# Kernel tuning notes

Measured on AMD Instinct MI355X. Metric: run time of the kernel, lower is better.

The kernel has to match this reference:

```python
import jax, jax.numpy as jnp
import numpy as np

DIM = 512
N_HEADS = 8
N_KV_HEADS = 4
HEAD_DIM = DIM // N_HEADS  # 64
N_REP = N_HEADS // N_KV_HEADS  # 2
THETA = 10000.0
EPS_RMS = 1e-6
EPS_Z = 1e-6


def setup_inputs() -> dict:
    key = jax.random.key(0)
    ks = jax.random.split(key, 6)
    s = 1.0 / np.sqrt(DIM)
    return {
        "x": jax.random.normal(ks[0], (4, 8192, DIM), dtype=jnp.float32),
        "norm_w": jnp.ones((DIM,), dtype=jnp.float32),
        "wq": jax.random.normal(ks[1], (DIM, DIM), dtype=jnp.float32) * s,
        "wk": jax.random.normal(ks[2], (N_KV_HEADS * HEAD_DIM, DIM), dtype=jnp.float32) * s,
        "wv": jax.random.normal(ks[3], (N_KV_HEADS * HEAD_DIM, DIM), dtype=jnp.float32) * s,
        "wo": jax.random.normal(ks[4], (DIM, DIM), dtype=jnp.float32) * s,
    }


def _rope_cos_sin(seq_len, head_dim):
    # freqs_cis = polar(1, t * theta^(-2i/d))
    inv = 1.0 / (THETA ** (jnp.arange(0, head_dim, 2, dtype=jnp.float32) / head_dim))
    ang = jnp.arange(seq_len, dtype=jnp.float32)[:, None] * inv[None, :]  # (S, d/2)
    return jnp.cos(ang), jnp.sin(ang)


def _apply_rope(t, cos, sin):
    # t: (B, S, H, d); complex rotation on consecutive pairs
    B, S, H, d = t.shape
    tr = t.reshape(B, S, H, d // 2, 2)
    xr, xi = tr[..., 0], tr[..., 1]
    c = cos[None, :, None, :]  # (1, S, 1, d/2)
    s = sin[None, :, None, :]
    out = jnp.stack([xr * c - xi * s, xr * s + xi * c], axis=-1)
    return out.reshape(B, S, H, d)


def _forward(x, norm_w, wq, wk, wv, wo):
    B, S, _ = x.shape
    # RMSNorm
    x = x * jax.lax.rsqrt(jnp.mean(x * x, axis=-1, keepdims=True) + EPS_RMS) * norm_w
    xq = (x @ wq.T).reshape(B, S, N_HEADS, HEAD_DIM)
    xk = (x @ wk.T).reshape(B, S, N_KV_HEADS, HEAD_DIM)
    xv = (x @ wv.T).reshape(B, S, N_KV_HEADS, HEAD_DIM)
    cos, sin = _rope_cos_sin(S, HEAD_DIM)
    xq = _apply_rope(xq, cos, sin)
    xk = _apply_rope(xk, cos, sin)
    # repeat_kv: (B,S,Hkv,d) -> (B,S,Hkv*n_rep,d)
    keys = jnp.repeat(xk, N_REP, axis=2)
    values = jnp.repeat(xv, N_REP, axis=2)
    # to (B, H, S, d)
    Q = jnp.transpose(xq, (0, 2, 1, 3))
    K = jnp.transpose(keys, (0, 2, 1, 3))
    V = jnp.transpose(values, (0, 2, 1, 3))
    phi = lambda t: jax.nn.elu(t) + 1.0
    Q_lin, K_lin = phi(Q), phi(K)
    # Faithful to source: elementwise product reduced over s -> (B,H,d)
    KV = jnp.einsum('bhsd,bhsd->bhd', K_lin, V)
    K_sum = K_lin.sum(axis=2)  # (B,H,d)
    Z = jnp.einsum('bhsd,bhd->bhs', Q_lin, K_sum)[..., None]  # (B,H,S,1)
    Y = Q_lin * KV[:, :, None, :] / (Z + EPS_Z)  # (B,H,S,d)
    Y = jnp.transpose(Y, (0, 2, 1, 3)).reshape(B, S, N_HEADS * HEAD_DIM)
    return Y @ wo.T


def reference(x, norm_w, wq, wk, wv, wo):
    return _forward(x, norm_w, wq, wk, wv, wo)
```

## Files before the change

### kernel.cpp

```cpp
#include <hip/hip_runtime.h>
#include <cmath>

typedef __attribute__((ext_vector_type(8))) short short8;
typedef __attribute__((ext_vector_type(4))) float floatx4;

#define T_TOK 32768
#define DIMK 512

__device__ __forceinline__ unsigned short f2bf(float f) {
  union { float f; unsigned int u; } v; v.f = f;
  unsigned int r = (v.u + 0x7fffu + ((v.u >> 16) & 1u)) >> 16;
  return (unsigned short)r;
}
__device__ __forceinline__ float bf2f(unsigned short h) {
  union { unsigned int u; float f; } v; v.u = ((unsigned int)h) << 16;
  return v.f;
}

__device__ __forceinline__ void gload_lds16(const unsigned short* g, unsigned short* ldsbase) {
  __builtin_amdgcn_global_load_lds(
      (const __attribute__((address_space(1))) unsigned int*)g,
      (__attribute__((address_space(3))) unsigned int*)ldsbase, 16, 0, 0);
}

__global__ __launch_bounds__(256) void k_prep(const float* __restrict__ x,
    const float* __restrict__ norm_w, const float* __restrict__ wq,
    const float* __restrict__ wk, const float* __restrict__ wv,
    const float* __restrict__ wo, unsigned short* __restrict__ Wb,
    unsigned short* __restrict__ wob, float2* __restrict__ rope,
    float* __restrict__ KVz, unsigned short* __restrict__ xn) {
  if (blockIdx.x < 2048) {
    int i = blockIdx.x * 256 + threadIdx.x;
    float v;
    if (i < 262144) {
      v = wq[i];
    } else {
      int R = i >> 9, col = i & 511;
      int h = (R - 512) >> 7, rem = (R - 512) & 127;
      if (rem < 64) v = wk[(h * 64 + rem) * 512 + col];
      else          v = wv[(h * 64 + rem - 64) * 512 + col];
    }
    Wb[i] = f2bf(v);
    if (i < 262144) {
      wob[i] = f2bf(wo[i]);
      int s = i >> 5, m = i & 31;
      const double c0 = 0.74989420933245582;
      double c1 = c0 * c0, c2 = c1 * c1, c3 = c2 * c2, c4 = c3 * c3;
      double p = 1.0;
      if (m & 1)  p *= c0;
      if (m & 2)  p *= c1;
      if (m & 4)  p *= c2;
      if (m & 8)  p *= c3;
      if (m & 16) p *= c4;
      double ang = (double)s * p;
      const double TWO_PI = 6.2831853071795864769;
      double q = rint(ang * (1.0 / TWO_PI));
      double r = fma(-q, TWO_PI, ang);
      float rf = (float)r;
      rope[i] = make_float2(cosf(rf), sinf(rf));
    }
    if (i < 2048) KVz[i] = 0.f;
  } else {
    int bid = blockIdx.x - 2048;
    int wave = threadIdx.x >> 6, lane = threadIdx.x & 63;
    size_t t0 = ((size_t)bid * 4 + wave) * 4;
    const float4* wr = (const float4*)norm_w;
    float4 w0 = wr[lane * 2], w1 = wr[lane * 2 + 1];
    float4 a[4], b[4];
    #pragma unroll
    for (int j = 0; j < 4; j++) {
      const float4* xr = (const float4*)(x + (t0 + j) * DIMK);
      a[j] = xr[lane * 2];
      b[j] = xr[lane * 2 + 1];
    }
    #pragma unroll
    for (int j = 0; j < 4; j++) {
      float ss = a[j].x * a[j].x + a[j].y * a[j].y + a[j].z * a[j].z + a[j].w * a[j].w
               + b[j].x * b[j].x + b[j].y * b[j].y + b[j].z * b[j].z + b[j].w * b[j].w;
      #pragma unroll
      for (int off = 32; off >= 1; off >>= 1) ss += __shfl_xor(ss, off, 64);
      float scale = rsqrtf(ss * (1.0f / DIMK) + 1e-6f);
      uint4 o;
      o.x = (unsigned int)f2bf(a[j].x * scale * w0.x) | ((unsigned int)f2bf(a[j].y * scale * w0.y) << 16);
      o.y = (unsigned int)f2bf(a[j].z * scale * w0.z) | ((unsigned int)f2bf(a[j].w * scale * w0.w) << 16);
      o.z = (unsigned int)f2bf(b[j].x * scale * w1.x) | ((unsigned int)f2bf(b[j].y * scale * w1.y) << 16);
      o.w = (unsigned int)f2bf(b[j].z * scale * w1.z) | ((unsigned int)f2bf(b[j].w * scale * w1.w) << 16);
      *(uint4*)(xn + (t0 + j) * DIMK + lane * 8) = o;
    }
  }
}

template <bool BF16_OUT, bool FUSE>
__global__ __launch_bounds__(512, 2) void k_gemm256(const unsigned short* __restrict__ A,
    const unsigned short* __restrict__ Bw, void* __restrict__ Cv, int ldc,
    const float2* __restrict__ rope, float* __restrict__ KV, float* __restrict__ Ksum) {
  constexpr int K = DIMK;
  extern __shared__ __align__(16) unsigned short smem[];
  unsigned short* const AsP = smem;
  unsigned short* const BsP = smem + 32768;

  const int tid = threadIdx.x;
  const int wave = tid >> 6, lane = tid & 63;
  const int r = lane & 15, quad = lane >> 4, r7 = r & 7;
  const int wm = (wave >> 2) * 128, wn = (wave & 3) * 64;

  const int nwg = gridDim.x * gridDim.y;
  const int bid = blockIdx.x + gridDim.x * blockIdx.y;
  const int cpx = nwg >> 3;
  const int nid = (bid & 7) * cpx + (bid >> 3);
  const int m0 = (nid & 127) * 256;
  const int n0 = (nid >> 7) * 256;

  const int srow = lane >> 3;
  const int scb = (lane & 7) ^ srow;
  const unsigned short* const Asrc = A + (size_t)(m0 + wave * 8 + srow) * K + scb * 8;
  const unsigned short* const Bsrc = Bw + (size_t)(n0 + wave * 8 + srow) * K + scb * 8;
  unsigned short* const Adst = AsP + wave * 8 * 64;
  unsigned short* const Bdst = BsP + wave * 8 * 64;

#define STAGE_A(buf, h, kt) do { \
    gload_lds16(Asrc + (size_t)((h) * 128) * K + (kt) * 64, Adst + (buf) * 16384 + ((h) * 128) * 64); \
    gload_lds16(Asrc + (size_t)((h) * 128 + 64) * K + (kt) * 64, Adst + (buf) * 16384 + ((h) * 128 + 64) * 64); \
  } while (0)
#define STAGE_B(buf, h, kt) do { \
    gload_lds16(Bsrc + (size_t)((h) * 128) * K + (kt) * 64, Bdst + (buf) * 16384 + ((h) * 128) * 64); \
    gload_lds16(Bsrc + (size_t)((h) * 128 + 64) * K + (kt) * 64, Bdst + (buf) * 16384 + ((h) * 128 + 64) * 64); \
  } while (0)

  short8 af[4][2], b0[2][2], b1[2][2];
  floatx4 acc[8][4];
  #pragma unroll
  for (int i = 0; i < 8; i++)
    #pragma unroll
    for (int jj = 0; jj < 4; jj++)
      acc[i][jj] = (floatx4){0.f, 0.f, 0.f, 0.f};

#define LDA8(buf, ah) do { \
    _Pragma("unroll") for (int ii = 0; ii < 4; ii++) \
      _Pragma("unroll") for (int kk = 0; kk < 2; kk++) \
        af[ii][kk] = *(const short8*)&AsP[(buf) * 16384 + (wm + (ah) * 64 + ii * 16 + r) * 64 + ((kk * 4 + quad) ^ r7) * 8]; \
  } while (0)
#define LDB4(buf, bh, arr) do { \
    _Pragma("unroll") for (int jj = 0; jj < 2; jj++) \
      _Pragma("unroll") for (int kk = 0; kk < 2; kk++) \
        arr[jj][kk] = *(const short8*)&BsP[(buf) * 16384 + (wn + (bh) * 32 + jj * 16 + r) * 64 + ((kk * 4 + quad) ^ r7) * 8]; \
  } while (0)
#define MFMAQ(ah, bh, arr) do { \
    __builtin_amdgcn_s_setprio(1); \
    _Pragma("unroll") for (int ii = 0; ii < 4; ii++) \
      _Pragma("unroll") for (int jj = 0; jj < 2; jj++) \
        _Pragma("unroll") for (int kk = 0; kk < 2; kk++) \
          acc[(ah) * 4 + ii][(bh) * 2 + jj] = __builtin_amdgcn_mfma_f32_16x16x32_bf16( \
              af[ii][kk], arr[jj][kk], acc[(ah) * 4 + ii][(bh) * 2 + jj], 0, 0, 0); \
    __builtin_amdgcn_s_setprio(0); \
  } while (0)
#define BAR() do { asm volatile("" ::: "memory"); __builtin_amdgcn_s_barrier(); asm volatile("" ::: "memory"); } while (0)
#define VMW(n) do { asm volatile("s_waitcnt vmcnt(" #n ")" ::: "memory"); __builtin_amdgcn_sched_barrier(0); } while (0)

  STAGE_A(0, 0, 0); STAGE_B(0, 0, 0); STAGE_A(0, 1, 0); STAGE_B(0, 1, 0);
  STAGE_A(1, 0, 1); STAGE_B(1, 0, 1); STAGE_A(1, 1, 1); STAGE_B(1, 1, 1);
  VMW(8);
  BAR();

  #pragma unroll
  for (int it = 0; it < 3; ++it) {
    const int kt = it * 2;
    LDA8(0, 0); LDB4(0, 0, b0);
    BAR(); MFMAQ(0, 0, b0); BAR();
    LDB4(0, 1, b1);
    BAR(); MFMAQ(0, 1, b1); BAR();
    LDA8(0, 1); STAGE_B(0, 0, kt + 2); STAGE_B(0, 1, kt + 2);
    BAR(); MFMAQ(1, 1, b1); BAR();
    STAGE_A(0, 0, kt + 2); STAGE_A(0, 1, kt + 2);
    BAR(); MFMAQ(1, 0, b0); VMW(8); BAR();
    LDA8(1, 0); LDB4(1, 0, b0);
    BAR(); MFMAQ(0, 0, b0); BAR();
    LDB4(1, 1, b1);
    BAR(); MFMAQ(0, 1, b1); BAR();
    LDA8(1, 1); STAGE_B(1, 0, kt + 3); STAGE_B(1, 1, kt + 3);
    BAR(); MFMAQ(1, 1, b1); BAR();
    STAGE_A(1, 0, kt + 3); STAGE_A(1, 1, kt + 3);
    BAR(); MFMAQ(1, 0, b0); VMW(8); BAR();
  }

  LDA8(0, 0); LDB4(0, 0, b0);
  BAR(); MFMAQ(0, 0, b0); BAR();
  LDB4(0, 1, b1);
  BAR(); MFMAQ(0, 1, b1); BAR();
  LDA8(0, 1);
  BAR(); MFMAQ(1, 1, b1); BAR();
  MFMAQ(1, 0, b0); VMW(0); BAR();
  LDA8(1, 0); LDB4(1, 0, b0);
  BAR(); MFMAQ(0, 0, b0); BAR();
  LDB4(1, 1, b1);
  BAR(); MFMAQ(0, 1, b1); BAR();
  LDA8(1, 1);
  BAR(); MFMAQ(1, 1, b1); BAR();
  MFMAQ(1, 0, b0);

  if (FUSE && n0 >= 512) {
#define VSW(t, d) ((t) * 128 + ((d) & 15) + (((((d) >> 4) + ((t) >> 2)) & 7) << 4))
    const int b = m0 >> 13;
    const int kh = ((n0 - 512) >> 8) * 2 + (wn >> 7);
    const int hvb = (wn >> 7) << 6;
    float* const Vs = (float*)smem;
    __syncthreads();
    if (wn & 64) {
      #pragma unroll
      for (int i = 0; i < 8; i++)
        #pragma unroll
        for (int j2 = 0; j2 < 4; j2++)
          #pragma unroll
          for (int p = 0; p < 4; p++) {
            int t = wm + i * 16 + quad * 4 + p;
            Vs[VSW(t, hvb + j2 * 16 + r)] = acc[i][j2][p];
          }
    }
    __syncthreads();
    if (!(wn & 64)) {
      float kvp[4] = {0.f, 0.f, 0.f, 0.f};
      float ksp[4] = {0.f, 0.f, 0.f, 0.f};
      #pragma unroll
      for (int i = 0; i < 8; i++)
        #pragma unroll
        for (int p = 0; p < 4; p++) {
          int t = wm + i * 16 + quad * 4 + p;
          int pos = (m0 + t) & 8191;
          #pragma unroll
          for (int j2 = 0; j2 < 4; j2++) {
            float v = acc[i][j2][p];
            float vp = __shfl_xor(v, 1, 64);
            int d = j2 * 16 + r;
            float2 cs = rope[pos * 32 + (d >> 1)];
            float rk = (r & 1) ? (vp * cs.y + v * cs.x) : (v * cs.x - vp * cs.y);
            rk = rk > 0.f ? rk + 1.f : __expf(rk);
            kvp[j2] += rk * Vs[VSW(t, hvb + d)];
            ksp[j2] += rk;
          }
        }
      #pragma unroll
      for (int j2 = 0; j2 < 4; j2++) {
        kvp[j2] += __shfl_xor(kvp[j2], 16, 64); kvp[j2] += __shfl_xor(kvp[j2], 32, 64);
        ksp[j2] += __shfl_xor(ksp[j2], 16, 64); ksp[j2] += __shfl_xor(ksp[j2], 32, 64);
      }
      if (lane < 16) {
        int base = (b * 4 + kh) * 64 + r;
        #pragma unroll
        for (int j2 = 0; j2 < 4; j2++) {
          atomicAdd(&KV[base + j2 * 16], kvp[j2]);
          atomicAdd(&Ksum[base + j2 * 16], ksp[j2]);
        }
      }
    }
#undef VSW
  } else {
    #pragma unroll
    for (int i = 0; i < 8; i++)
      #pragma unroll
      for (int j2 = 0; j2 < 4; j2++) {
        int row = m0 + wm + i * 16 + quad * 4;
        int col = n0 + wn + j2 * 16 + r;
        #pragma unroll
        for (int p = 0; p < 4; p++) {
          if constexpr (BF16_OUT) {
            ((unsigned short*)Cv)[(size_t)(row + p) * ldc + col] = f2bf(acc[i][j2][p]);
          } else {
            ((float*)Cv)[(size_t)(row + p) * ldc + col] = acc[i][j2][p];
          }
        }
      }
  }
#undef STAGE_A
#undef STAGE_B
#undef LDA8
#undef LDB4
#undef MFMAQ
#undef BAR
#undef VMW
}

__global__ __launch_bounds__(256) void k_qkern(const unsigned short* __restrict__ qkv,
    const float2* __restrict__ rope, const float* __restrict__ KV,
    const float* __restrict__ Ksum, unsigned short* __restrict__ Yb) {
  const int h = threadIdx.x >> 5;
  const int pr = threadIdx.x & 31;
  const int t0 = blockIdx.x * 8;
  const int b = t0 >> 13;
  const int bk = b * 4 + (h >> 1);
  const float2 ks = *(const float2*)(Ksum + bk * 64 + 2 * pr);
  const float2 kv = *(const float2*)(KV + bk * 64 + 2 * pr);
  unsigned int qp[8]; float2 cs[8];
  #pragma unroll
  for (int j = 0; j < 8; j++) {
    int t = t0 + j;
    qp[j] = *(const unsigned int*)(qkv + (size_t)t * 512 + h * 64 + 2 * pr);
    cs[j] = rope[(t & 8191) * 32 + pr];
  }
  float ar[8], ai[8], z[8];
  #pragma unroll
  for (int j = 0; j < 8; j++) {
    float qx = bf2f((unsigned short)(qp[j] & 0xffffu));
    float qy = bf2f((unsigned short)(qp[j] >> 16));
    float a = qx * cs[j].x - qy * cs[j].y;
    float i2 = qx * cs[j].y + qy * cs[j].x;
    a  = a  > 0.f ? a  + 1.f : __expf(a);
    i2 = i2 > 0.f ? i2 + 1.f : __expf(i2);
    ar[j] = a; ai[j] = i2;
    z[j] = a * ks.x + i2 * ks.y;
  }
  #pragma unroll
  for (int off = 16; off >= 1; off >>= 1)
    #pragma unroll
    for (int j = 0; j < 8; j++)
      z[j] += __shfl_xor(z[j], off, 64);
  #pragma unroll
  for (int j = 0; j < 8; j++) {
    float inv = 1.0f / (z[j] + 1e-6f);
    unsigned int o = (unsigned int)f2bf(ar[j] * kv.x * inv)
                   | ((unsigned int)f2bf(ai[j] * kv.y * inv) << 16);
    *(unsigned int*)(Yb + (size_t)(t0 + j) * 512 + h * 64 + 2 * pr) = o;
  }
}

extern "C" void kernel_launch(void* const* d_in, const int* in_sizes, int n_in,
                              void* d_out, int out_size, void* d_ws, size_t ws_size,
                              hipStream_t stream) {
  const float* x = (const float*)d_in[0];
  const float* norm_w = (const float*)d_in[1];
  const float* wq = (const float*)d_in[2];
  const float* wk = (const float*)d_in[3];
  const float* wv = (const float*)d_in[4];
  const float* wo = (const float*)d_in[5];
  float* out = (float*)d_out;

  char* ws = (char*)d_ws;
  unsigned short* xn  = (unsigned short*)(ws);
  unsigned short* Wb  = (unsigned short*)(ws + 33554432);
  unsigned short* wob = (unsigned short*)(ws + 34603008);
  unsigned short* qkv = (unsigned short*)(ws + 35127296);
  float2* rope        = (float2*)(ws + 102236160);
  float* KV           = (float*)(ws + 104333312);
  float* Ksum         = (float*)(ws + 104337408);
  unsigned short* Yb  = (unsigned short*)(ws);

  static bool s_attr = false;
  if (!s_attr) {
    (void)hipFuncSetAttribute(reinterpret_cast<const void*>(&k_gemm256<true, true>),
                              hipFuncAttributeMaxDynamicSharedMemorySize, 131072);
    (void)hipFuncSetAttribute(reinterpret_cast<const void*>(&k_gemm256<false, false>),
                              hipFuncAttributeMaxDynamicSharedMemorySize, 131072);
    s_attr = true;
  }

  k_prep<<<4096, 256, 0, stream>>>(x, norm_w, wq, wk, wv, wo, Wb, wob, rope, KV, xn);
  k_gemm256<true, true><<<dim3(128, 4), 512, 131072, stream>>>(
      xn, Wb, (void*)qkv, 512, rope, KV, Ksum);
  k_qkern<<<4096, 256, 0, stream>>>(qkv, rope, KV, Ksum, Yb);
  k_gemm256<false, false><<<dim3(128, 2), 512, 131072, stream>>>(
      Yb, wob, (void*)out, 512, nullptr, nullptr, nullptr);
}
```

Measured before the change: 207.2 us.

## Fuse Q feature-map normalization into output projection GEMM A-tile staging

```diff
diff --git a/kernel.cpp b/kernel.cpp
--- a/kernel.cpp
+++ b/kernel.cpp
@@ -279,47 +279,191 @@
 #undef VMW
 }
 
-__global__ __launch_bounds__(256) void k_qkern(const unsigned short* __restrict__ qkv,
-    const float2* __restrict__ rope, const float* __restrict__ KV,
-    const float* __restrict__ Ksum, unsigned short* __restrict__ Yb) {
-  const int h = threadIdx.x >> 5;
-  const int pr = threadIdx.x & 31;
-  const int t0 = blockIdx.x * 8;
-  const int b = t0 >> 13;
-  const int bk = b * 4 + (h >> 1);
-  const float2 ks = *(const float2*)(Ksum + bk * 64 + 2 * pr);
-  const float2 kv = *(const float2*)(KV + bk * 64 + 2 * pr);
-  unsigned int qp[8]; float2 cs[8];
+__global__ __launch_bounds__(512, 2) void k_gemm2q(const unsigned short* __restrict__ Aq,
+    const unsigned short* __restrict__ Bw, float* __restrict__ Cv,
+    const float* __restrict__ ropef, const float* __restrict__ KV,
+    const float* __restrict__ Ksum) {
+  constexpr int K = DIMK;
+  extern __shared__ __align__(16) unsigned short smem[];
+  unsigned short* const AsP = smem;
+  unsigned short* const BsP = smem + 32768;
+
+  const int tid = threadIdx.x;
+  const int wave = tid >> 6, lane = tid & 63;
+  const int r = lane & 15, quad = lane >> 4, r7 = r & 7;
+  const int wm = (wave >> 2) * 128, wn = (wave & 3) * 64;
+  const int srow = lane >> 3, cc = lane & 7;
+  const int scb = cc ^ srow;
+
+  const int nwg = gridDim.x * gridDim.y;
+  const int bid = blockIdx.x + gridDim.x * blockIdx.y;
+  const int cpx = nwg >> 3;
+  const int nid = (bid & 7) * cpx + (bid >> 3);
+  const int m0 = (nid & 127) * 256;
+  const int n0 = (nid >> 7) * 256;
+  const int bq = m0 >> 13;
+  const int d0 = cc * 8;
+
+  const unsigned short* const Bsrc = Bw + (size_t)(n0 + wave * 8 + srow) * K + scb * 8;
+  unsigned short* const Bdst = BsP + wave * 8 * 64;
+
+#define BSTG(buf, kt) do { \
+    gload_lds16(Bsrc + (size_t)0 * K + (kt) * 64, Bdst + (buf) * 16384 + 0 * 64); \
+    gload_lds16(Bsrc + (size_t)64 * K + (kt) * 64, Bdst + (buf) * 16384 + 64 * 64); \
+    gload_lds16(Bsrc + (size_t)128 * K + (kt) * 64, Bdst + (buf) * 16384 + 128 * 64); \
+    gload_lds16(Bsrc + (size_t)192 * K + (kt) * 64, Bdst + (buf) * 16384 + 192 * 64); \
+  } while (0)
+
+  float4 rp[8];
+  uint4 qreg[4];
+  float4 kvA, kvB, ksA, ksB;
   #pragma unroll
-  for (int j = 0; j < 8; j++) {
-    int t = t0 + j;
-    qp[j] = *(const unsigned int*)(qkv + (size_t)t * 512 + h * 64 + 2 * pr);
-    cs[j] = rope[(t & 8191) * 32 + pr];
+  for (int ss = 0; ss < 4; ss++) {
+    int R = (ss >> 1) * 128 + (ss & 1) * 64 + wave * 8 + srow;
+    int pos = (m0 + R) & 8191;
+    rp[ss * 2]     = *(const float4*)(ropef + (size_t)pos * 64 + cc * 8);
+    rp[ss * 2 + 1] = *(const float4*)(ropef + (size_t)pos * 64 + cc * 8 + 4);
   }
-  float ar[8], ai[8], z[8];
+
+#define QLOAD(kt) do { \
+    const int bk_ = bq * 4 + ((kt) >> 1); \
+    kvA = *(const float4*)(KV + bk_ * 64 + d0); \
+    kvB = *(const float4*)(KV + bk_ * 64 + d0 + 4); \
+    ksA = *(const float4*)(Ksum + bk_ * 64 + d0); \
+    ksB = *(const float4*)(Ksum + bk_ * 64 + d0 + 4); \
+    _Pragma("unroll") for (int ss = 0; ss < 4; ss++) { \
+      int R_ = (ss >> 1) * 128 + (ss & 1) * 64 + wave * 8 + srow; \
+      qreg[ss] = *(const uint4*)(Aq + (size_t)(m0 + R_) * 512 + (kt) * 64 + d0); \
+    } \
+  } while (0)
+
+#define PH(x) ((x) > 0.f ? (x) + 1.f : __expf(x))
+
+#define QWRITE(buf) do { \
+    _Pragma("unroll") for (int ss = 0; ss < 4; ss++) { \
+      int R_ = (ss >> 1) * 128 + (ss & 1) * 64 + wave * 8 + srow; \
+      float q0 = bf2f((unsigned short)(qreg[ss].x & 0xffffu)); \
+      float q1 = bf2f((unsigned short)(qreg[ss].x >> 16)); \
+      float q2 = bf2f((unsigned short)(qreg[ss].y & 0xffffu)); \
+      float q3 = bf2f((unsigned short)(qreg[ss].y >> 16)); \
+      float q4 = bf2f((unsigned short)(qreg[ss].z & 0xffffu)); \
+      float q5 = bf2f((unsigned short)(qreg[ss].z >> 16)); \
+      float q6 = bf2f((unsigned short)(qreg[ss].w & 0xffffu)); \
+      float q7 = bf2f((unsigned short)(qreg[ss].w >> 16)); \
+      float4 ra = rp[ss * 2], rb = rp[ss * 2 + 1]; \
+      float p0 = PH(q0 * ra.x - q1 * ra.y), p1 = PH(q0 * ra.y + q1 * ra.x); \
+      float p2 = PH(q2 * ra.z - q3 * ra.w), p3 = PH(q2 * ra.w + q3 * ra.z); \
+      float p4 = PH(q4 * rb.x - q5 * rb.y), p5 = PH(q4 * rb.y + q5 * rb.x); \
+      float p6 = PH(q6 * rb.z - q7 * rb.w), p7 = PH(q6 * rb.w + q7 * rb.z); \
+      float zp = p0 * ksA.x + p1 * ksA.y + p2 * ksA.z + p3 * ksA.w \
+               + p4 * ksB.x + p5 * ksB.y + p6 * ksB.z + p7 * ksB.w; \
+      zp += __shfl_xor(zp, 1, 64); \
+      zp += __shfl_xor(zp, 2, 64); \
+      zp += __shfl_xor(zp, 4, 64); \
+      float inv_ = 1.0f / (zp + 1e-6f); \
+      uint4 o_; \
+      o_.x = (unsigned int)f2bf(p0 * kvA.x * inv_) | ((unsigned int)f2bf(p1 * kvA.y * inv_) << 16); \
+      o_.y = (unsigned int)f2bf(p2 * kvA.z * inv_) | ((unsigned int)f2bf(p3 * kvA.w * inv_) << 16); \
+      o_.z = (unsigned int)f2bf(p4 * kvB.x * inv_) | ((unsigned int)f2bf(p5 * kvB.y * inv_) << 16); \
+      o_.w = (unsigned int)f2bf(p6 * kvB.z * inv_) | ((unsigned int)f2bf(p7 * kvB.w * inv_) << 16); \
+      *(uint4*)&AsP[(buf) * 16384 + R_ * 64 + (cc ^ srow) * 8] = o_; \
+    } \
+  } while (0)
+
+  short8 af[4][2], b0[2][2], b1[2][2];
+  floatx4 acc[8][4];
   #pragma unroll
-  for (int j = 0; j < 8; j++) {
-    float qx = bf2f((unsigned short)(qp[j] & 0xffffu));
-    float qy = bf2f((unsigned short)(qp[j] >> 16));
-    float a = qx * cs[j].x - qy * cs[j].y;
-    float i2 = qx * cs[j].y + qy * cs[j].x;
-    a  = a  > 0.f ? a  + 1.f : __expf(a);
-    i2 = i2 > 0.f ? i2 + 1.f : __expf(i2);
-    ar[j] = a; ai[j] = i2;
-    z[j] = a * ks.x + i2 * ks.y;
+  for (int i = 0; i < 8; i++)
+    #pragma unroll
+    for (int jj = 0; jj < 4; jj++)
+      acc[i][jj] = (floatx4){0.f, 0.f, 0.f, 0.f};
+
+#define LDA8(buf, ah) do { \
+    _Pragma("unroll") for (int ii = 0; ii < 4; ii++) \
+      _Pragma("unroll") for (int kk = 0; kk < 2; kk++) \
+        af[ii][kk] = *(const short8*)&AsP[(buf) * 16384 + (wm + (ah) * 64 + ii * 16 + r) * 64 + ((kk * 4 + quad) ^ r7) * 8]; \
+  } while (0)
+#define LDB4(buf, bh, arr) do { \
+    _Pragma("unroll") for (int jj = 0; jj < 2; jj++) \
+      _Pragma("unroll") for (int kk = 0; kk < 2; kk++) \
+        arr[jj][kk] = *(const short8*)&BsP[(buf) * 16384 + (wn + (bh) * 32 + jj * 16 + r) * 64 + ((kk * 4 + quad) ^ r7) * 8]; \
+  } while (0)
+#define MFMAQ(ah, bh, arr) do { \
+    __builtin_amdgcn_s_setprio(1); \
+    _Pragma("unroll") for (int ii = 0; ii < 4; ii++) \
+      _Pragma("unroll") for (int jj = 0; jj < 2; jj++) \
+        _Pragma("unroll") for (int kk = 0; kk < 2; kk++) \
+          acc[(ah) * 4 + ii][(bh) * 2 + jj] = __builtin_amdgcn_mfma_f32_16x16x32_bf16( \
+              af[ii][kk], arr[jj][kk], acc[(ah) * 4 + ii][(bh) * 2 + jj], 0, 0, 0); \
+    __builtin_amdgcn_s_setprio(0); \
+  } while (0)
+#define BAR() do { asm volatile("" ::: "memory"); __builtin_amdgcn_s_barrier(); asm volatile("" ::: "memory"); } while (0)
+#define VMW(n) do { asm volatile("s_waitcnt vmcnt(" #n ")" ::: "memory"); __builtin_amdgcn_sched_barrier(0); } while (0)
+#define LGKM() do { asm volatile("s_waitcnt lgkmcnt(0)" ::: "memory"); __builtin_amdgcn_sched_barrier(0); } while (0)
+
+  BSTG(0, 0); BSTG(1, 1);
+  QLOAD(0); QWRITE(0);
+  QLOAD(1); QWRITE(1);
+  LGKM();
+  VMW(4);
+  BAR();
+
+  #pragma unroll
+  for (int it = 0; it < 3; ++it) {
+    const int kt = it * 2;
+    LDA8(0, 0); LDB4(0, 0, b0); QLOAD(kt + 2);
+    BAR(); MFMAQ(0, 0, b0); BAR();
+    LDB4(0, 1, b1);
+    BAR(); MFMAQ(0, 1, b1); BAR();
+    LDA8(0, 1); BSTG(0, kt + 2);
+    BAR(); MFMAQ(1, 1, b1); BAR();
+    QWRITE(0);
+    LGKM(); BAR(); MFMAQ(1, 0, b0); VMW(4); BAR();
+    LDA8(1, 0); LDB4(1, 0, b0); QLOAD(kt + 3);
+    BAR(); MFMAQ(0, 0, b0); BAR();
+    LDB4(1, 1, b1);
+    BAR(); MFMAQ(0, 1, b1); BAR();
+    LDA8(1, 1); BSTG(1, kt + 3);
+    BAR(); MFMAQ(1, 1, b1); BAR();
+    QWRITE(1);
+    LGKM(); BAR(); MFMAQ(1, 0, b0); VMW(4); BAR();
   }
+
+  LDA8(0, 0); LDB4(0, 0, b0);
+  BAR(); MFMAQ(0, 0, b0); BAR();
+  LDB4(0, 1, b1);
+  BAR(); MFMAQ(0, 1, b1); BAR();
+  LDA8(0, 1);
+  BAR(); MFMAQ(1, 1, b1); BAR();
+  MFMAQ(1, 0, b0); VMW(0); BAR();
+  LDA8(1, 0); LDB4(1, 0, b0);
+  BAR(); MFMAQ(0, 0, b0); BAR();
+  LDB4(1, 1, b1);
+  BAR(); MFMAQ(0, 1, b1); BAR();
+  LDA8(1, 1);
+  BAR(); MFMAQ(1, 1, b1); BAR();
+  MFMAQ(1, 0, b0);
+
   #pragma unroll
-  for (int off = 16; off >= 1; off >>= 1)
+  for (int i = 0; i < 8; i++)
     #pragma unroll
-    for (int j = 0; j < 8; j++)
-      z[j] += __shfl_xor(z[j], off, 64);
-  #pragma unroll
-  for (int j = 0; j < 8; j++) {
-    float inv = 1.0f / (z[j] + 1e-6f);
-    unsigned int o = (unsigned int)f2bf(ar[j] * kv.x * inv)
-                   | ((unsigned int)f2bf(ai[j] * kv.y * inv) << 16);
-    *(unsigned int*)(Yb + (size_t)(t0 + j) * 512 + h * 64 + 2 * pr) = o;
-  }
+    for (int j2 = 0; j2 < 4; j2++) {
+      int row = m0 + wm + i * 16 + quad * 4;
+      int col = n0 + wn + j2 * 16 + r;
+      #pragma unroll
+      for (int p = 0; p < 4; p++)
+        Cv[(size_t)(row + p) * 512 + col] = acc[i][j2][p];
+    }
+#undef BSTG
+#undef QLOAD
+#undef PH
+#undef QWRITE
+#undef LDA8
+#undef LDB4
+#undef MFMAQ
+#undef BAR
+#undef VMW
+#undef LGKM
 }
 
 extern "C" void kernel_launch(void* const* d_in, const int* in_sizes, int n_in,
@@ -341,13 +485,12 @@
   float2* rope        = (float2*)(ws + 102236160);
   float* KV           = (float*)(ws + 104333312);
   float* Ksum         = (float*)(ws + 104337408);
-  unsigned short* Yb  = (unsigned short*)(ws);
 
   static bool s_attr = false;
   if (!s_attr) {
     (void)hipFuncSetAttribute(reinterpret_cast<const void*>(&k_gemm256<true, true>),
                               hipFuncAttributeMaxDynamicSharedMemorySize, 131072);
-    (void)hipFuncSetAttribute(reinterpret_cast<const void*>(&k_gemm256<false, false>),
+    (void)hipFuncSetAttribute(reinterpret_cast<const void*>(&k_gemm2q),
                               hipFuncAttributeMaxDynamicSharedMemorySize, 131072);
     s_attr = true;
   }
@@ -355,7 +498,6 @@
   k_prep<<<4096, 256, 0, stream>>>(x, norm_w, wq, wk, wv, wo, Wb, wob, rope, KV, xn);
   k_gemm256<true, true><<<dim3(128, 4), 512, 131072, stream>>>(
       xn, Wb, (void*)qkv, 512, rope, KV, Ksum);
-  k_qkern<<<4096, 256, 0, stream>>>(qkv, rope, KV, Ksum, Yb);
-  k_gemm256<false, false><<<dim3(128, 2), 512, 131072, stream>>>(
-      Yb, wob, (void*)out, 512, nullptr, nullptr, nullptr);
-}
+  k_gemm2q<<<dim3(128, 2), 512, 131072, stream>>>(
+      qkv, wob, out, (const float*)rope, KV, Ksum);
+}
```

Result: slower. 276.0 us (+33.2%).
